# Performance work log

Measured on AMD Instinct MI355X. Metric: run time of the kernel, lower is better.

The kernel has to match this reference:

```python
import jax, jax.numpy as jnp
import numpy as np
from jax import lax

N_OBJ = 21   # 20 VOC classes + background
N_ACT = 27   # HICO actions
HUMAN = 14   # index of 'human' in VOC_BBOX_LABEL_NAMES
ROI_SZ = 7
SCALE = 1.0 / 16.0
STD = (0.1, 0.1, 0.2, 0.2)
MEAN = (0.0, 0.0, 0.0, 0.0)
SIGMA = 0.3
NMS_T = 0.0  # thresh passed to non_maximum_suppression in source
EPS = 1e-3
NEG = -1e30


def setup_inputs():
    key = jax.random.key(0)
    ks = jax.random.split(key, 9)
    R = 2000
    C, Hf, Wf = 512, 38, 50
    Himg, Wimg = 608, 800
    x = jax.random.normal(ks[0], (1, C, Hf, Wf), dtype=jnp.float32)
    pred_scores = jax.random.normal(ks[1], (R, N_OBJ), dtype=jnp.float32)
    pred_off = 0.5 * jax.random.normal(ks[2], (R, N_OBJ * 4), dtype=jnp.float32)
    ys = jnp.sort(jax.random.uniform(ks[3], (R, 2), minval=0.0, maxval=Himg - 1.0), axis=1)
    xs = jnp.sort(jax.random.uniform(ks[4], (R, 2), minval=0.0, maxval=Wimg - 1.0), axis=1)
    rois = jnp.stack([ys[:, 0], xs[:, 0], ys[:, 1] + 1.0, xs[:, 1] + 1.0], axis=1)  # [R,4] yxyx, image coords
    D = C * ROI_SZ * ROI_SZ  # 25088
    W1 = jax.random.normal(ks[5], (D, 4096), dtype=jnp.float32) / np.float32(np.sqrt(D))
    b1 = jnp.zeros((4096,), jnp.float32)
    W2 = jax.random.normal(ks[6], (4096, 4096), dtype=jnp.float32) / 64.0
    b2 = jnp.zeros((4096,), jnp.float32)
    W_loc = jax.random.normal(ks[7], (4096, 4), dtype=jnp.float32) / 64.0
    b_loc = jnp.zeros((4,), jnp.float32)
    W_act = jax.random.normal(ks[8], (4096, N_ACT), dtype=jnp.float32) / 64.0
    b_act = jnp.zeros((N_ACT,), jnp.float32)
    imgshape = jnp.array([Himg, Wimg], dtype=jnp.int32)
    return {"x": x, "pred_scores": pred_scores, "pred_off": pred_off, "rois": rois,
            "imgshape": imgshape, "W1": W1, "b1": b1, "W2": W2, "b2": b2,
            "W_loc": W_loc, "b_loc": b_loc, "W_act": W_act, "b_act": b_act}


def loc2bbox(src, loc):
    # src, loc: [...,4] (y1,x1,y2,x2) / (dy,dx,dh,dw)
    h = src[..., 2] - src[..., 0]
    w = src[..., 3] - src[..., 1]
    cy = src[..., 0] + 0.5 * h
    cx = src[..., 1] + 0.5 * w
    cy2 = loc[..., 0] * h + cy
    cx2 = loc[..., 1] * w + cx
    h2 = jnp.exp(loc[..., 2]) * h
    w2 = jnp.exp(loc[..., 3]) * w
    return jnp.stack([cy2 - 0.5 * h2, cx2 - 0.5 * w2, cy2 + 0.5 * h2, cx2 + 0.5 * w2], axis=-1)


def nms_keep(boxes, scores):
    # chainercv-style greedy NMS: suppress if IoU with an already-kept box >= NMS_T
    R = boxes.shape[0]
    order = jnp.argsort(-scores)
    b = boxes[order]
    tl = jnp.maximum(b[:, None, :2], b[None, :, :2])
    br = jnp.minimum(b[:, None, 2:], b[None, :, 2:])
    inter = jnp.prod(jnp.maximum(br - tl, 0.0), axis=-1)
    area = jnp.prod(jnp.maximum(b[:, 2:] - b[:, :2], 0.0), axis=-1)
    iou = inter / (area[:, None] + area[None, :] - inter + 1e-12)
    idx = jnp.arange(R)
    def body(i, keep):
        sup = jnp.any((iou[i] >= NMS_T) & keep & (idx < i))
        return keep.at[i].set(~sup)
    keep_sorted = lax.fori_loop(0, R, body, jnp.ones((R,), bool))
    return jnp.zeros((R,), bool).at[order].set(keep_sorted)


def roi_pool(feat, box_yxyx):
    # chainer RoIPooling2D on one roi; roi fed as [x1,y1,x2,y2] then scaled by SCALE
    C, Hf, Wf = feat.shape
    y1, x1, y2, x2 = box_yxyx[0], box_yxyx[1], box_yxyx[2], box_yxyx[3]
    xmin = jnp.round(x1 * SCALE).astype(jnp.int32)
    ymin = jnp.round(y1 * SCALE).astype(jnp.int32)
    xmax = jnp.round(x2 * SCALE).astype(jnp.int32)
    ymax = jnp.round(y2 * SCALE).astype(jnp.int32)
    rw = jnp.maximum(xmax - xmin + 1, 1).astype(jnp.float32)
    rh = jnp.maximum(ymax - ymin + 1, 1).astype(jnp.float32)
    p = jnp.arange(ROI_SZ, dtype=jnp.float32)
    hstart = jnp.clip(ymin + jnp.floor(p * rh / ROI_SZ).astype(jnp.int32), 0, Hf)
    hend = jnp.clip(ymin + jnp.ceil((p + 1.0) * rh / ROI_SZ).astype(jnp.int32), 0, Hf)
    wstart = jnp.clip(xmin + jnp.floor(p * rw / ROI_SZ).astype(jnp.int32), 0, Wf)
    wend = jnp.clip(xmin + jnp.ceil((p + 1.0) * rw / ROI_SZ).astype(jnp.int32), 0, Wf)
    r = jnp.arange(Hf)
    c = jnp.arange(Wf)
    rowm = (r[None, :] >= hstart[:, None]) & (r[None, :] < hend[:, None])  # [7,Hf]
    colm = (c[None, :] >= wstart[:, None]) & (c[None, :] < wend[:, None])  # [7,Wf]
    t = jnp.where(colm[None, None, :, :], feat[:, :, None, :], NEG).max(axis=-1)  # [C,Hf,7]
    out = jnp.where(rowm[None, :, :, None], t[:, None, :, :], NEG).max(axis=2)    # [C,7,7]
    return jnp.where(out <= NEG * 0.5, 0.0, out)


def xywh(b):
    # quirky encoding used in forward: x=(b3-b1)/2, y=(b2-b0)/2, w=b3-b1, h=b2-b0
    w = b[..., 3] - b[..., 1]
    h = b[..., 2] - b[..., 0]
    return jnp.stack([0.5 * w, 0.5 * h, w, h], axis=-1)


def reference(x, pred_scores, pred_off, rois, imgshape, W1, b1, W2, b2, W_loc, b_loc, W_act, b_act):
    Hf, Wf = x.shape[2], x.shape[3]
    R = rois.shape[0]
    img = imgshape.astype(jnp.float32)
    my_scale = Hf / img[0]
    sy = Hf / img[0]
    sx = Wf / img[1]
    roi = rois * jnp.stack([sy, sx, sy, sx])  # resize_bbox(image -> feature)
    std = jnp.tile(jnp.asarray(STD, jnp.float32), (N_OBJ,))
    mean = jnp.tile(jnp.asarray(MEAN, jnp.float32), (N_OBJ,))
    loc = (pred_off * std + mean).reshape(R, N_OBJ, 4)
    src = jnp.broadcast_to(roi[:, None, :], loc.shape)
    cb = loc2bbox(src, loc)  # [R,21,4]
    yc = jnp.clip(cb[..., 0::2], 0.0, float(Hf))
    xc = jnp.clip(cb[..., 1::2], 0.0, float(Wf))
    cls_bbox = jnp.stack([yc[..., 0], xc[..., 0], yc[..., 1], xc[..., 1]], axis=-1)
    prob = jax.nn.softmax(pred_scores, axis=1)  # strictly > 0, so prob>0 mask keeps all
    boxes_c = jnp.swapaxes(cls_bbox[:, 1:, :], 0, 1)  # [20,R,4]
    scores_c = prob[:, 1:].T                          # [20,R]
    keep = jax.vmap(nms_keep)(boxes_c, scores_c)      # [20,R] bool
    bbox_all = boxes_c.reshape(-1, 4)
    score_all = scores_c.reshape(-1)
    label_all = jnp.repeat(jnp.arange(N_OBJ - 1), R)
    kept = keep.reshape(-1)
    # get_pred_human_box: best-scoring kept box with label 'human'
    hmask = kept & (label_all == HUMAN)
    hi = jnp.argmax(jnp.where(hmask, score_all, -1.0))
    human_box = bbox_all[hi]  # feature coords, yxyx
    # RoI pool + classifier heads
    pool = roi_pool(x[0], human_box)
    feat = pool.reshape(1, -1)  # [1, 25088]
    fc7 = jax.nn.relu(jax.nn.relu(feat @ W1 + b1) @ W2 + b2)
    pred_object_loc = fc7 @ W_loc + b_loc   # [1,4]
    action_scores = fc7 @ W_act + b_act     # [1,27]
    # test-mode: gaussian over relative box encodings to pick object
    h4 = xywh(human_box)
    mu = xywh(pred_object_loc[0])
    cand = xywh(bbox_all)  # [20R,4]
    hw = jnp.maximum(h4[2], EPS)
    hh = jnp.maximum(h4[3], EPS)
    cw = jnp.maximum(cand[:, 2], EPS)
    ch = jnp.maximum(cand[:, 3], EPS)
    boh = jnp.stack([(cand[:, 0] - h4[0]) / hw, (cand[:, 1] - h4[1]) / hh,
                     jnp.log(cw / hw), jnp.log(ch / hh)], axis=-1)
    gau = jnp.exp(-jnp.sum((boh - mu) ** 2, axis=-1) / (2.0 * SIGMA * SIGMA))
    vmask = kept & (label_all != HUMAN)
    bi = jnp.argmax(jnp.where(vmask, gau, -1.0))
    obj_box = bbox_all[bi]
    # resize back to image coords (flip_bbox treated as identity)
    inv = jnp.stack([img[0] / Hf, img[1] / Wf, img[0] / Hf, img[1] / Wf])
    pred_human_box = (human_box * inv)[None, :]
    pred_obj_box = (obj_box * inv)[None, :]
    return pred_human_box, pred_obj_box, action_scores, my_scale
```

## Files before the change

### kernel.cpp

```cpp
#include <hip/hip_runtime.h>
#include <math.h>

#define R_ROIS 2000
#define NOBJ   21
#define NACT   27
#define HUMAN  14
#define CFEAT  512
#define HF     38
#define WF     50
#define DFEAT  (CFEAT*7*7)
#define H1DIM  4096

#define WS_LOGZ   0
#define WS_KEPT   2000
#define WS_FEAT   2080
#define WS_H1     27168
#define WS_H1R    31264
#define WS_FC7    35360
#define WS_FC7R   39456
#define WS_LOC    43552
#define WS_ACT    43556

__global__ void k_init(float* h1, float* fc7) {
    int i = blockIdx.x * blockDim.x + threadIdx.x;
    if (i < H1DIM) { h1[i] = 0.f; fc7[i] = 0.f; }
}

__global__ void k_logz(const float* __restrict__ scores, float* __restrict__ logZ) {
    int r = blockIdx.x * blockDim.x + threadIdx.x;
    if (r >= R_ROIS) return;
    const float* s = scores + r * NOBJ;
    float m = s[0];
    #pragma unroll
    for (int c = 1; c < NOBJ; ++c) m = fmaxf(m, s[c]);
    float sum = 0.f;
    #pragma unroll
    for (int c = 0; c < NOBJ; ++c) sum += expf(s[c] - m);
    logZ[r] = m + logf(sum);
}

__global__ void k_class_top(const float* __restrict__ scores, const float* __restrict__ logZ,
                            const float* __restrict__ off, const float* __restrict__ rois,
                            const int* __restrict__ imgshape, float* __restrict__ kept_box) {
    int cls = blockIdx.x + 1;
    __shared__ float sval[256];
    __shared__ int   sidx[256];
    float best = -1e30f; int bidx = 0x7fffffff;
    for (int r = threadIdx.x; r < R_ROIS; r += 256) {
        float v = scores[r * NOBJ + cls] - logZ[r];
        if (v > best) { best = v; bidx = r; }
    }
    sval[threadIdx.x] = best; sidx[threadIdx.x] = bidx;
    __syncthreads();
    for (int s = 128; s > 0; s >>= 1) {
        if (threadIdx.x < s) {
            float ov = sval[threadIdx.x + s]; int oi = sidx[threadIdx.x + s];
            if (ov > sval[threadIdx.x] ||
                (ov == sval[threadIdx.x] && oi < sidx[threadIdx.x])) {
                sval[threadIdx.x] = ov; sidx[threadIdx.x] = oi;
            }
        }
        __syncthreads();
    }
    if (threadIdx.x == 0) {
        int r = sidx[0];
        float Himg = (float)imgshape[0], Wimg = (float)imgshape[1];
        float sy = (float)HF / Himg, sx = (float)WF / Wimg;
        float y1 = rois[r*4+0]*sy, x1 = rois[r*4+1]*sx;
        float y2 = rois[r*4+2]*sy, x2 = rois[r*4+3]*sx;
        float dy = off[r*(NOBJ*4) + cls*4+0] * 0.1f;
        float dx = off[r*(NOBJ*4) + cls*4+1] * 0.1f;
        float dh = off[r*(NOBJ*4) + cls*4+2] * 0.2f;
        float dw = off[r*(NOBJ*4) + cls*4+3] * 0.2f;
        float h = y2 - y1, w = x2 - x1;
        float cy = y1 + 0.5f*h, cx = x1 + 0.5f*w;
        float cy2 = dy*h + cy, cx2 = dx*w + cx;
        float h2 = expf(dh)*h, w2 = expf(dw)*w;
        float by1 = fminf(fmaxf(cy2 - 0.5f*h2, 0.f), (float)HF);
        float bx1 = fminf(fmaxf(cx2 - 0.5f*w2, 0.f), (float)WF);
        float by2 = fminf(fmaxf(cy2 + 0.5f*h2, 0.f), (float)HF);
        float bx2 = fminf(fmaxf(cx2 + 0.5f*w2, 0.f), (float)WF);
        int l = cls - 1;
        kept_box[l*4+0] = by1; kept_box[l*4+1] = bx1;
        kept_box[l*4+2] = by2; kept_box[l*4+3] = bx2;
    }
}

__global__ void k_roipool(const float* __restrict__ x, const float* __restrict__ kept_box,
                          float* __restrict__ feat) {
    int idx = blockIdx.x * blockDim.x + threadIdx.x;
    if (idx >= DFEAT) return;
    float y1 = kept_box[HUMAN*4+0], x1 = kept_box[HUMAN*4+1];
    float y2 = kept_box[HUMAN*4+2], x2 = kept_box[HUMAN*4+3];
    int xmin = (int)rintf(x1 * 0.0625f);
    int ymin = (int)rintf(y1 * 0.0625f);
    int xmax = (int)rintf(x2 * 0.0625f);
    int ymax = (int)rintf(y2 * 0.0625f);
    float rw = (float)max(xmax - xmin + 1, 1);
    float rh = (float)max(ymax - ymin + 1, 1);
    int c = idx / 49, rem = idx % 49, pi = rem / 7, pj = rem % 7;
    int hs  = min(max(ymin + (int)floorf((float)pi * rh / 7.f), 0), HF);
    int he  = min(max(ymin + (int)ceilf((float)(pi+1) * rh / 7.f), 0), HF);
    int wss = min(max(xmin + (int)floorf((float)pj * rw / 7.f), 0), WF);
    int we  = min(max(xmin + (int)ceilf((float)(pj+1) * rw / 7.f), 0), WF);
    float m = -1e30f;
    for (int rr = hs; rr < he; ++rr)
        for (int cc = wss; cc < we; ++cc)
            m = fmaxf(m, x[c*(HF*WF) + rr*WF + cc]);
    feat[idx] = (m <= -5e29f) ? 0.f : m;
}

template<int ROWS>
__global__ __launch_bounds__(256)
void k_matvec(const float* __restrict__ W, const float* __restrict__ vin,
              float* __restrict__ vout, int ncols) {
    __shared__ float sv[ROWS];
    int row0 = blockIdx.x * ROWS;
    int col0 = blockIdx.y * 1024 + threadIdx.x * 4;
    for (int i = threadIdx.x; i < ROWS; i += 256) sv[i] = vin[row0 + i];
    __syncthreads();
    float a0 = 0.f, a1 = 0.f, a2 = 0.f, a3 = 0.f;
    const float4* Wv = (const float4*)W;
    long base = ((long)row0 * ncols + col0) >> 2;
    int stride = ncols >> 2;
    #pragma unroll 4
    for (int i = 0; i < ROWS; ++i) {
        float f = sv[i];
        float4 w = Wv[base + (long)i * stride];
        a0 += f * w.x; a1 += f * w.y; a2 += f * w.z; a3 += f * w.w;
    }
    atomicAdd(&vout[col0+0], a0);
    atomicAdd(&vout[col0+1], a1);
    atomicAdd(&vout[col0+2], a2);
    atomicAdd(&vout[col0+3], a3);
}

__global__ void k_bias_relu(const float* __restrict__ vin, const float* __restrict__ b,
                            float* __restrict__ vout, int n) {
    int i = blockIdx.x * blockDim.x + threadIdx.x;
    if (i < n) vout[i] = fmaxf(vin[i] + b[i], 0.f);
}

__global__ void k_heads(const float* __restrict__ fc7r,
                        const float* __restrict__ W_loc, const float* __restrict__ b_loc,
                        const float* __restrict__ W_act, const float* __restrict__ b_act,
                        float* __restrict__ loc_out, float* __restrict__ act_out) {
    int k = blockIdx.x;
    __shared__ float red[256];
    float sum = 0.f;
    if (k < 4) {
        for (int i = threadIdx.x; i < H1DIM; i += 256) sum += fc7r[i] * W_loc[i*4 + k];
    } else {
        int j = k - 4;
        for (int i = threadIdx.x; i < H1DIM; i += 256) sum += fc7r[i] * W_act[i*NACT + j];
    }
    red[threadIdx.x] = sum; __syncthreads();
    for (int s = 128; s > 0; s >>= 1) {
        if (threadIdx.x < s) red[threadIdx.x] += red[threadIdx.x + s];
        __syncthreads();
    }
    if (threadIdx.x == 0) {
        if (k < 4) loc_out[k] = red[0] + b_loc[k];
        else       act_out[k-4] = red[0] + b_act[k-4];
    }
}

__global__ void k_final(const float* __restrict__ kept_box, const float* __restrict__ loc_out,
                        const float* __restrict__ act_out, const int* __restrict__ imgshape,
                        float* __restrict__ out) {
    if (threadIdx.x != 0 || blockIdx.x != 0) return;
    float hb0 = kept_box[HUMAN*4+0], hb1 = kept_box[HUMAN*4+1];
    float hb2 = kept_box[HUMAN*4+2], hb3 = kept_box[HUMAN*4+3];
    float h4w = hb3 - hb1, h4h = hb2 - hb0;
    float h4x = 0.5f * h4w, h4y = 0.5f * h4h;
    float hw = fmaxf(h4w, 1e-3f), hh = fmaxf(h4h, 1e-3f);
    float l0 = loc_out[0], l1 = loc_out[1], l2 = loc_out[2], l3 = loc_out[3];
    float muw = l3 - l1, muh = l2 - l0;
    float mux = 0.5f * muw, muy = 0.5f * muh;
    float bestg = -2.f; int bl = 0;
    for (int l = 0; l < 20; ++l) {
        if (l == HUMAN) continue;
        float b0 = kept_box[l*4+0], b1 = kept_box[l*4+1];
        float b2 = kept_box[l*4+2], b3 = kept_box[l*4+3];
        float cw = fmaxf(b3 - b1, 1e-3f), ch = fmaxf(b2 - b0, 1e-3f);
        float c0 = 0.5f * (b3 - b1), c1 = 0.5f * (b2 - b0);
        float d0 = (c0 - h4x) / hw - mux;
        float d1 = (c1 - h4y) / hh - muy;
        float d2 = logf(cw / hw) - muw;
        float d3 = logf(ch / hh) - muh;
        float g = expf(-(d0*d0 + d1*d1 + d2*d2 + d3*d3) / (2.f * 0.3f * 0.3f));
        if (g > bestg) { bestg = g; bl = l; }
    }
    float Himg = (float)imgshape[0], Wimg = (float)imgshape[1];
    float iy = Himg / (float)HF, ix = Wimg / (float)WF;
    out[0] = hb0 * iy; out[1] = hb1 * ix; out[2] = hb2 * iy; out[3] = hb3 * ix;
    out[4] = kept_box[bl*4+0] * iy; out[5] = kept_box[bl*4+1] * ix;
    out[6] = kept_box[bl*4+2] * iy; out[7] = kept_box[bl*4+3] * ix;
    for (int j = 0; j < NACT; ++j) out[8+j] = act_out[j];
    out[35] = (float)HF / Himg;
}

extern "C" void kernel_launch(void* const* d_in, const int* in_sizes, int n_in,
                              void* d_out, int out_size, void* d_ws, size_t ws_size,
                              hipStream_t stream) {
    const float* x           = (const float*)d_in[0];
    const float* pred_scores = (const float*)d_in[1];
    const float* pred_off    = (const float*)d_in[2];
    const float* rois        = (const float*)d_in[3];
    const int*   imgshape    = (const int*)d_in[4];
    const float* W1          = (const float*)d_in[5];
    const float* b1          = (const float*)d_in[6];
    const float* W2          = (const float*)d_in[7];
    const float* b2          = (const float*)d_in[8];
    const float* W_loc       = (const float*)d_in[9];
    const float* b_loc       = (const float*)d_in[10];
    const float* W_act       = (const float*)d_in[11];
    const float* b_act       = (const float*)d_in[12];
    float* out = (float*)d_out;

    float* ws   = (float*)d_ws;
    float* logZ = ws + WS_LOGZ;
    float* kept = ws + WS_KEPT;
    float* feat = ws + WS_FEAT;
    float* h1   = ws + WS_H1;
    float* h1r  = ws + WS_H1R;
    float* fc7  = ws + WS_FC7;
    float* fc7r = ws + WS_FC7R;
    float* loco = ws + WS_LOC;
    float* acto = ws + WS_ACT;

    k_init<<<16, 256, 0, stream>>>(h1, fc7);
    k_logz<<<(R_ROIS + 255) / 256, 256, 0, stream>>>(pred_scores, logZ);
    k_class_top<<<20, 256, 0, stream>>>(pred_scores, logZ, pred_off, rois, imgshape, kept);
    k_roipool<<<(DFEAT + 255) / 256, 256, 0, stream>>>(x, kept, feat);
    k_matvec<128><<<dim3(196, 4), 256, 0, stream>>>(W1, feat, h1, H1DIM);
    k_bias_relu<<<16, 256, 0, stream>>>(h1, b1, h1r, H1DIM);
    k_matvec<64><<<dim3(64, 4), 256, 0, stream>>>(W2, h1r, fc7, H1DIM);
    k_bias_relu<<<16, 256, 0, stream>>>(fc7, b2, fc7r, H1DIM);
    k_heads<<<31, 256, 0, stream>>>(fc7r, W_loc, b_loc, W_act, b_act, loco, acto);
    k_final<<<1, 64, 0, stream>>>(kept, loco, acto, imgshape, out);
}
```

Before: 635.2 us.

## Replace atomic matvec accumulation with partial-sum buffers and fused reduce

The matvec kernels now write per-row-block partial sums to workspace instead of using atomicAdd. A separate reduce kernel sums the partials and applies bias and ReLU, so the init and bias_relu kernels are no longer needed. Each thread now handles two float4 column groups, and the W2 split uses 128 row blocks of 32 rows to raise parallelism. The log-softmax normaliser is computed inline inside class_top, which drops the logz kernel but makes each of the 20 class blocks recompute it. In exchange there is extra workspace traffic for the partial buffers (196x4096 and 128x4096 floats) and a reduce pass over them.

```diff
diff --git a/kernel.cpp b/kernel.cpp
--- a/kernel.cpp
+++ b/kernel.cpp
@@ -10,36 +10,20 @@
 #define WF     50
 #define DFEAT  (CFEAT*7*7)
 #define H1DIM  4096
-
-#define WS_LOGZ   0
-#define WS_KEPT   2000
-#define WS_FEAT   2080
-#define WS_H1     27168
-#define WS_H1R    31264
-#define WS_FC7    35360
-#define WS_FC7R   39456
-#define WS_LOC    43552
-#define WS_ACT    43556
-
-__global__ void k_init(float* h1, float* fc7) {
-    int i = blockIdx.x * blockDim.x + threadIdx.x;
-    if (i < H1DIM) { h1[i] = 0.f; fc7[i] = 0.f; }
-}
-
-__global__ void k_logz(const float* __restrict__ scores, float* __restrict__ logZ) {
-    int r = blockIdx.x * blockDim.x + threadIdx.x;
-    if (r >= R_ROIS) return;
-    const float* s = scores + r * NOBJ;
-    float m = s[0];
-    #pragma unroll
-    for (int c = 1; c < NOBJ; ++c) m = fmaxf(m, s[c]);
-    float sum = 0.f;
-    #pragma unroll
-    for (int c = 0; c < NOBJ; ++c) sum += expf(s[c] - m);
-    logZ[r] = m + logf(sum);
-}
-
-__global__ void k_class_top(const float* __restrict__ scores, const float* __restrict__ logZ,
+#define NC     4096
+#define NP1    196
+#define NP2    128
+
+#define WS_KEPT   0
+#define WS_FEAT   128
+#define WS_P1     25216
+#define WS_H1R    (WS_P1 + NP1*NC)
+#define WS_P2     (WS_H1R + NC)
+#define WS_FC7R   (WS_P2 + NP2*NC)
+#define WS_LOC    (WS_FC7R + NC)
+#define WS_ACT    (WS_LOC + 4)
+
+__global__ void k_class_top(const float* __restrict__ scores,
                             const float* __restrict__ off, const float* __restrict__ rois,
                             const int* __restrict__ imgshape, float* __restrict__ kept_box) {
     int cls = blockIdx.x + 1;
@@ -47,7 +31,14 @@
     __shared__ int   sidx[256];
     float best = -1e30f; int bidx = 0x7fffffff;
     for (int r = threadIdx.x; r < R_ROIS; r += 256) {
-        float v = scores[r * NOBJ + cls] - logZ[r];
+        const float* s = scores + r * NOBJ;
+        float m = s[0];
+        #pragma unroll
+        for (int c = 1; c < NOBJ; ++c) m = fmaxf(m, s[c]);
+        float sum = 0.f;
+        #pragma unroll
+        for (int c = 0; c < NOBJ; ++c) sum += expf(s[c] - m);
+        float v = s[cls] - (m + logf(sum));
         if (v > best) { best = v; bidx = r; }
     }
     sval[threadIdx.x] = best; sidx[threadIdx.x] = bidx;
@@ -112,33 +103,35 @@
 
 template<int ROWS>
 __global__ __launch_bounds__(256)
-void k_matvec(const float* __restrict__ W, const float* __restrict__ vin,
-              float* __restrict__ vout, int ncols) {
+void k_mv_part(const float* __restrict__ W, const float* __restrict__ vin,
+               float* __restrict__ part) {
     __shared__ float sv[ROWS];
     int row0 = blockIdx.x * ROWS;
-    int col0 = blockIdx.y * 1024 + threadIdx.x * 4;
+    int col0 = blockIdx.y * 2048 + threadIdx.x * 4;
     for (int i = threadIdx.x; i < ROWS; i += 256) sv[i] = vin[row0 + i];
     __syncthreads();
-    float a0 = 0.f, a1 = 0.f, a2 = 0.f, a3 = 0.f;
+    float a0=0.f,a1=0.f,a2=0.f,a3=0.f,b0=0.f,b1=0.f,b2=0.f,b3=0.f;
     const float4* Wv = (const float4*)W;
-    long base = ((long)row0 * ncols + col0) >> 2;
-    int stride = ncols >> 2;
+    long base = ((long)row0 * NC + col0) >> 2;
     #pragma unroll 4
     for (int i = 0; i < ROWS; ++i) {
         float f = sv[i];
-        float4 w = Wv[base + (long)i * stride];
-        a0 += f * w.x; a1 += f * w.y; a2 += f * w.z; a3 += f * w.w;
-    }
-    atomicAdd(&vout[col0+0], a0);
-    atomicAdd(&vout[col0+1], a1);
-    atomicAdd(&vout[col0+2], a2);
-    atomicAdd(&vout[col0+3], a3);
-}
-
-__global__ void k_bias_relu(const float* __restrict__ vin, const float* __restrict__ b,
-                            float* __restrict__ vout, int n) {
-    int i = blockIdx.x * blockDim.x + threadIdx.x;
-    if (i < n) vout[i] = fmaxf(vin[i] + b[i], 0.f);
+        float4 w0 = Wv[base + (long)i * (NC/4)];
+        float4 w1 = Wv[base + (long)i * (NC/4) + 256];
+        a0 += f*w0.x; a1 += f*w0.y; a2 += f*w0.z; a3 += f*w0.w;
+        b0 += f*w1.x; b1 += f*w1.y; b2 += f*w1.z; b3 += f*w1.w;
+    }
+    float4* p = (float4*)(part + (long)blockIdx.x * NC + col0);
+    p[0]   = make_float4(a0, a1, a2, a3);
+    p[256] = make_float4(b0, b1, b2, b3);
+}
+
+__global__ void k_reduce(const float* __restrict__ part, const float* __restrict__ bias,
+                         float* __restrict__ vout, int nparts) {
+    int c = blockIdx.x * 256 + threadIdx.x;
+    float s = 0.f;
+    for (int p = 0; p < nparts; ++p) s += part[(long)p * NC + c];
+    vout[c] = fmaxf(s + bias[c], 0.f);
 }
 
 __global__ void k_heads(const float* __restrict__ fc7r,
@@ -219,24 +212,21 @@
     float* out = (float*)d_out;
 
     float* ws   = (float*)d_ws;
-    float* logZ = ws + WS_LOGZ;
     float* kept = ws + WS_KEPT;
     float* feat = ws + WS_FEAT;
-    float* h1   = ws + WS_H1;
+    float* p1   = ws + WS_P1;
     float* h1r  = ws + WS_H1R;
-    float* fc7  = ws + WS_FC7;
+    float* p2   = ws + WS_P2;
     float* fc7r = ws + WS_FC7R;
     float* loco = ws + WS_LOC;
     float* acto = ws + WS_ACT;
 
-    k_init<<<16, 256, 0, stream>>>(h1, fc7);
-    k_logz<<<(R_ROIS + 255) / 256, 256, 0, stream>>>(pred_scores, logZ);
-    k_class_top<<<20, 256, 0, stream>>>(pred_scores, logZ, pred_off, rois, imgshape, kept);
+    k_class_top<<<20, 256, 0, stream>>>(pred_scores, pred_off, rois, imgshape, kept);
     k_roipool<<<(DFEAT + 255) / 256, 256, 0, stream>>>(x, kept, feat);
-    k_matvec<128><<<dim3(196, 4), 256, 0, stream>>>(W1, feat, h1, H1DIM);
-    k_bias_relu<<<16, 256, 0, stream>>>(h1, b1, h1r, H1DIM);
-    k_matvec<64><<<dim3(64, 4), 256, 0, stream>>>(W2, h1r, fc7, H1DIM);
-    k_bias_relu<<<16, 256, 0, stream>>>(fc7, b2, fc7r, H1DIM);
+    k_mv_part<128><<<dim3(NP1, 2), 256, 0, stream>>>(W1, feat, p1);
+    k_reduce<<<16, 256, 0, stream>>>(p1, b1, h1r, NP1);
+    k_mv_part<32><<<dim3(NP2, 2), 256, 0, stream>>>(W2, h1r, p2);
+    k_reduce<<<16, 256, 0, stream>>>(p2, b2, fc7r, NP2);
     k_heads<<<31, 256, 0, stream>>>(fc7r, W_loc, b_loc, W_act, b_act, loco, acto);
     k_final<<<1, 64, 0, stream>>>(kept, loco, acto, imgshape, out);
 }
```

Result: slower. 711.1 us (+11.9%).
